# Optimization experiments

Hardware: AMD Instinct MI355X
Metric: run time of the kernel (lower is better)

## Reference

```python
import jax, jax.numpy as jnp
import numpy as np

N = 100000      # nodes
E = 3200000     # edges (avg degree 32)
F_IN = 256      # n_features
HID = 128       # n_hidden
C = 16          # n_classes
K = 10          # propagation hops


def setup_inputs() -> dict:
    key = jax.random.key(0)
    ks = jax.random.split(key, 12)
    x = jax.random.normal(ks[0], (N, F_IN), jnp.float32)
    edge_index = jax.random.randint(ks[1], (2, E), 0, N, dtype=jnp.int64)
    edge_attr = jax.random.uniform(ks[2], (E,), jnp.float32)
    # learned parameters (torch Linear layout: W [out, in], b [out])
    def lin(k, fan_out, fan_in):
        s = 1.0 / np.sqrt(fan_in)
        kw, kb = jax.random.split(k)
        W = jax.random.uniform(kw, (fan_out, fan_in), jnp.float32, -s, s)
        b = jax.random.uniform(kb, (fan_out,), jnp.float32, -s, s)
        return W, b
    lin1_w, lin1_b = lin(ks[3], HID, F_IN)
    lin2_w, lin2_b = lin(ks[4], HID, HID)   # hidden lin (n_layers-3 == 1)
    lin3_w, lin3_b = lin(ks[5], C, HID)     # classes lin
    proj_w, proj_b = lin(ks[6], 1, C)       # Prop retain-score projection
    return {"x": x, "edge_index": edge_index, "edge_attr": edge_attr,
            "lin1_w": lin1_w, "lin1_b": lin1_b,
            "lin2_w": lin2_w, "lin2_b": lin2_b,
            "lin3_w": lin3_w, "lin3_b": lin3_b,
            "proj_w": proj_w, "proj_b": proj_b}


def reference(x, edge_index, edge_attr,
              lin1_w, lin1_b, lin2_w, lin2_b, lin3_w, lin3_b,
              proj_w, proj_b):
    # MLP stack (dropout is identity in eval mode)
    h = jax.nn.relu(x @ lin1_w.T + lin1_b)
    h = jax.nn.relu(h @ lin2_w.T + lin2_b)
    h = jax.nn.relu(h @ lin3_w.T + lin3_b)          # [N, C]

    src, dst = edge_index[0], edge_index[1]
    norm = edge_attr[:, None]                        # [E, 1]

    def hop(carry, _):
        msg = norm * carry[src]                      # gather + scale [E, C]
        nxt = jax.ops.segment_sum(msg, dst, num_segments=N)  # scatter-add
        return nxt, nxt

    _, hops = jax.lax.scan(hop, h, None, length=K)   # [K, N, C]
    pps = jnp.concatenate([h[None], hops], axis=0)   # [K+1, N, C]
    pps = jnp.transpose(pps, (1, 0, 2))              # [N, K+1, C]

    # adaptive combination: sigmoid(Linear(C->1)) per hop, weighted sum
    score = jax.nn.sigmoid(jnp.einsum('nkc,c->nk', pps, proj_w[0]) + proj_b[0])
    out = jnp.einsum('nk,nkc->nc', score, pps)       # [N, C]
    return out
```

## Files before the change

kernel.cpp:

```cpp
#include <hip/hip_runtime.h>
#include <hip/hip_bf16.h>
#include <math.h>

#define N_NODES 100000
#define E_EDGES 3200000
#define K_HOPS  10
#define NPP     256
#define NPART   ((N_NODES + NPP - 1) / NPP)
#define CHUNK   4096
#define EPT     (CHUNK / 256)
#define NCHUNK  ((E_EDGES + CHUNK - 1) / CHUNK)
#define NFLAT   (NPART * NCHUNK)
#define SSEG    8192
#define GA      ((NFLAT + SSEG - 1) / SSEG)

typedef __attribute__((ext_vector_type(8))) short short8;
typedef __attribute__((ext_vector_type(4))) float floatx4;

__device__ __forceinline__ ushort f2bf(float f) {
    uint u = __float_as_uint(f);
    u += 0x7fffu + ((u >> 16) & 1u);
    return (ushort)(u >> 16);
}
__device__ __forceinline__ uint pk2(float a, float b) {
    return (uint)f2bf(a) | ((uint)f2bf(b) << 16);
}
__device__ __forceinline__ float bflo(uint u) { return __uint_as_float(u << 16); }
__device__ __forceinline__ float bfhi(uint u) { return __uint_as_float(u & 0xffff0000u); }

template<int KD, int MD, bool A_F32>
__global__ __launch_bounds__(256) void mfma_mlp(
    const void* __restrict__ Av, const float* __restrict__ W,
    const float* __restrict__ bias, ushort* __restrict__ C)
{
    constexpr int NCT = MD / 16;
    constexpr int LDW = 88;
    __shared__ ushort Wl[MD * LDW];

    const int t    = threadIdx.x;
    const int w    = t >> 6;
    const int lane = t & 63;
    const int m    = lane & 15;
    const int quad = lane >> 4;
    const int rowBase = blockIdx.x * 128 + w * 32;

    floatx4 acc[2][NCT];
#pragma unroll
    for (int rt = 0; rt < 2; ++rt)
#pragma unroll
        for (int ct = 0; ct < NCT; ++ct) acc[rt][ct] = (floatx4)0.f;

    for (int kb = 0; kb < KD; kb += 64) {
#pragma unroll
        for (int j = 0; j < MD / 16; ++j) {
            int flat = j * 256 + t;
            int n  = flat >> 4;
            int c4 = (flat & 15) * 4;
            floatx4 v = *(const floatx4*)&W[(size_t)n * KD + kb + c4];
            *(uint2*)&Wl[n * LDW + c4] = make_uint2(pk2(v[0], v[1]), pk2(v[2], v[3]));
        }
        __syncthreads();
#pragma unroll
        for (int ks = 0; ks < 64; ks += 32) {
            short8 af[2];
#pragma unroll
            for (int rt = 0; rt < 2; ++rt) {
                int row = rowBase + rt * 16 + m;
                row = row < N_NODES ? row : N_NODES - 1;
                size_t base = (size_t)row * KD + kb + ks + quad * 8;
                if constexpr (A_F32) {
                    const float* ap = (const float*)Av + base;
                    floatx4 a0 = *(const floatx4*)ap;
                    floatx4 a1 = *(const floatx4*)(ap + 4);
                    short8 x;
                    x[0] = (short)f2bf(a0[0]); x[1] = (short)f2bf(a0[1]);
                    x[2] = (short)f2bf(a0[2]); x[3] = (short)f2bf(a0[3]);
                    x[4] = (short)f2bf(a1[0]); x[5] = (short)f2bf(a1[1]);
                    x[6] = (short)f2bf(a1[2]); x[7] = (short)f2bf(a1[3]);
                    af[rt] = x;
                } else {
                    af[rt] = *(const short8*)((const ushort*)Av + base);
                }
            }
#pragma unroll
            for (int ct = 0; ct < NCT; ++ct) {
                short8 bf = *(const short8*)&Wl[(ct * 16 + m) * LDW + ks + quad * 8];
#pragma unroll
                for (int rt = 0; rt < 2; ++rt)
                    acc[rt][ct] = __builtin_amdgcn_mfma_f32_16x16x32_bf16(
                        af[rt], bf, acc[rt][ct], 0, 0, 0);
            }
        }
        __syncthreads();
    }

#pragma unroll
    for (int rt = 0; rt < 2; ++rt) {
#pragma unroll
        for (int r = 0; r < 4; ++r) {
            int row = rowBase + rt * 16 + quad * 4 + r;
            if (row < N_NODES) {
#pragma unroll
                for (int ct = 0; ct < NCT; ++ct) {
                    int col = ct * 16 + m;
                    float v = acc[rt][ct][r] + bias[col];
                    v = v > 0.f ? v : 0.f;
                    C[(size_t)row * MD + col] = f2bf(v);
                }
            }
        }
    }
}

__global__ __launch_bounds__(256) void hist2(
    const int* __restrict__ dst, int* __restrict__ cmat)
{
    __shared__ int lhist[NPART];
    const int t = threadIdx.x;
    for (int p = t; p < NPART; p += 256) lhist[p] = 0;
    __syncthreads();
    const int base = blockIdx.x * CHUNK;
#pragma unroll
    for (int j = 0; j < EPT; ++j) {
        int i = base + j * 256 + t;
        if (i < E_EDGES) atomicAdd(&lhist[dst[i] >> 8], 1);
    }
    __syncthreads();
    for (int p = t; p < NPART; p += 256)
        cmat[p * NCHUNK + blockIdx.x] = lhist[p];
}

__global__ __launch_bounds__(1024) void scan_reduce(
    const int* __restrict__ cmat, int* __restrict__ bsum)
{
    __shared__ int wsum[16];
    const int t = threadIdx.x, lane = t & 63, wid = t >> 6;
    int base = blockIdx.x * SSEG + t * 8;
    int s = 0;
#pragma unroll
    for (int j = 0; j < 8; ++j) {
        int idx = base + j;
        if (idx < NFLAT) s += cmat[idx];
    }
#pragma unroll
    for (int d = 1; d < 64; d <<= 1) s += __shfl_xor(s, d);
    if (lane == 0) wsum[wid] = s;
    __syncthreads();
    if (t == 0) {
        int tot = 0;
#pragma unroll
        for (int i = 0; i < 16; ++i) tot += wsum[i];
        bsum[blockIdx.x] = tot;
    }
}

__global__ void scan_tops(const int* __restrict__ bsum, int* __restrict__ boff)
{
    const int t = threadIdx.x;
    int v = (t < GA) ? bsum[t] : 0;
    int x = v;
#pragma unroll
    for (int d = 1; d < 64; d <<= 1) {
        int y = __shfl_up(x, d);
        if (t >= d) x += y;
    }
    if (t < GA) boff[t] = x - v;
}

__global__ __launch_bounds__(1024) void scan_apply(
    int* __restrict__ cmat, const int* __restrict__ boff, int* __restrict__ pbase)
{
    __shared__ int wsum[16];
    __shared__ int woff[17];
    const int t = threadIdx.x, lane = t & 63, wid = t >> 6;
    int base = blockIdx.x * SSEG + t * 8;
    int v[8], pre[8];
    int s = 0;
#pragma unroll
    for (int j = 0; j < 8; ++j) {
        int idx = base + j;
        v[j] = (idx < NFLAT) ? cmat[idx] : 0;
        pre[j] = s;
        s += v[j];
    }
    int x = s;
#pragma unroll
    for (int d = 1; d < 64; d <<= 1) {
        int y = __shfl_up(x, d);
        if (lane >= d) x += y;
    }
    if (lane == 63) wsum[wid] = x;
    __syncthreads();
    if (wid == 0) {
        int w = (lane < 16) ? wsum[lane] : 0;
#pragma unroll
        for (int d = 1; d < 16; d <<= 1) {
            int y = __shfl_up(w, d);
            if (lane >= d) w += y;
        }
        if (lane < 16) woff[lane + 1] = w;
        if (lane == 0) woff[0] = 0;
    }
    __syncthreads();
    int tbase = boff[blockIdx.x] + woff[wid] + (x - s);
#pragma unroll
    for (int j = 0; j < 8; ++j) {
        int idx = base + j;
        if (idx < NFLAT) {
            int e = tbase + pre[j];
            cmat[idx] = e;
            if (idx % NCHUNK == 0) pbase[idx / NCHUNK] = e;
        }
    }
    if (blockIdx.x == 0 && t == 0) pbase[NPART] = E_EDGES;
}

__global__ __launch_bounds__(256) void scatter2(
    const int* __restrict__ src, const int* __restrict__ dst,
    const float* __restrict__ ea, const int* __restrict__ cbase,
    int2* __restrict__ staging)
{
    __shared__ int lcur[NPART];
    const int t = threadIdx.x;
    const int b = blockIdx.x;
    for (int p = t; p < NPART; p += 256) lcur[p] = cbase[p * NCHUNK + b];
    __syncthreads();
    const int base = b * CHUNK;

    int d[EPT], pos[EPT];
#pragma unroll
    for (int j = 0; j < EPT; ++j) {
        int i = base + j * 256 + t;
        d[j] = (i < E_EDGES) ? dst[i] : -1;
    }
#pragma unroll
    for (int j = 0; j < EPT; ++j) {
        if (d[j] >= 0) pos[j] = atomicAdd(&lcur[d[j] >> 8], 1);
    }
#pragma unroll
    for (int j = 0; j < EPT; ++j) {
        if (d[j] >= 0) {
            int i = base + j * 256 + t;
            staging[pos[j]] = make_int2(__float_as_int(ea[i]),
                                        src[i] | ((d[j] & 255) << 17));
        }
    }
}

__global__ __launch_bounds__(1024) void partition_build(
    const int2* __restrict__ staging, const int* __restrict__ pbase,
    int* __restrict__ rowp, int2* __restrict__ csr)
{
    __shared__ int ncnt[NPP];
    __shared__ int wsum[4];
    const int p = blockIdx.x;
    const int t = threadIdx.x;
    const int e0 = pbase[p], e1 = pbase[p + 1];
    const int cnt = e1 - e0;
    const int n0 = p << 8;

    if (t < NPP) ncnt[t] = 0;
    __syncthreads();
    for (int e = t; e < cnt; e += 1024)
        atomicAdd(&ncnt[(staging[e0 + e].y >> 17) & 255], 1);
    __syncthreads();

    int x = 0, v = 0;
    if (t < NPP) {
        const int lane = t & 63, wid = t >> 6;
        v = ncnt[t];
        x = v;
#pragma unroll
        for (int d = 1; d < 64; d <<= 1) {
            int y = __shfl_up(x, d);
            if (lane >= d) x += y;
        }
        if (lane == 63) wsum[wid] = x;
    }
    __syncthreads();
    if (t < NPP) {
        const int wid = t >> 6;
        int wbase = 0;
#pragma unroll
        for (int w = 0; w < 4; ++w) if (w < wid) wbase += wsum[w];
        int excl = wbase + x - v;
        ncnt[t] = e0 + excl;
        int n = n0 + t;
        if (n < N_NODES) rowp[n] = e0 + excl;
    }
    if (p == NPART - 1 && t == 0) rowp[N_NODES] = E_EDGES;
    __syncthreads();

    for (int e = t; e < cnt; e += 1024) {
        int2 en = staging[e0 + e];
        int dlo = (en.y >> 17) & 255;
        int pos = atomicAdd(&ncnt[dlo], 1);
        csr[pos] = make_int2(en.y & 0x1FFFF, en.x);
    }
}

__global__ __launch_bounds__(256) void init_out_bf16(
    const ushort* __restrict__ h, const float* __restrict__ pw,
    const float* __restrict__ pb, float* __restrict__ out)
{
    const int t = threadIdx.x;
    const int l = t & 1;
    const int n = blockIdx.x * 128 + (t >> 1);
    if (n >= N_NODES) return;
    uint4 v = *(const uint4*)&h[(size_t)n * 16 + l * 8];
    float a0 = bflo(v.x), a1 = bfhi(v.x), a2 = bflo(v.y), a3 = bfhi(v.y);
    float a4 = bflo(v.z), a5 = bfhi(v.z), a6 = bflo(v.w), a7 = bfhi(v.w);
    float4 p0 = ((const float4*)pw)[l * 2];
    float4 p1 = ((const float4*)pw)[l * 2 + 1];
    float part = a0 * p0.x + a1 * p0.y + a2 * p0.z + a3 * p0.w
               + a4 * p1.x + a5 * p1.y + a6 * p1.z + a7 * p1.w;
    part += __shfl_xor(part, 1);
    float s = 1.f / (1.f + __expf(-(part + pb[0])));
    *(float4*)&out[(size_t)n * 16 + l * 8]     = make_float4(s*a0, s*a1, s*a2, s*a3);
    *(float4*)&out[(size_t)n * 16 + l * 8 + 4] = make_float4(s*a4, s*a5, s*a6, s*a7);
}

__global__ __launch_bounds__(256) void hop_bf16(
    const ushort* __restrict__ prev, ushort* __restrict__ next,
    const int* __restrict__ rowp, const int2* __restrict__ csr,
    const float* __restrict__ pw, const float* __restrict__ pb,
    float* __restrict__ out)
{
    const int t = threadIdx.x;
    const int l = t & 1;
    const int g = (t >> 1) & 3;
    const int n = blockIdx.x * 32 + (t >> 3);
    if (n >= N_NODES) return;
    const int e0 = rowp[n], e1 = rowp[n + 1];
    float a[8];
#pragma unroll
    for (int j = 0; j < 8; ++j) a[j] = 0.f;

    int e = e0 + g;
    for (; e + 4 < e1; e += 8) {
        int2 c0 = csr[e];
        int2 c1 = csr[e + 4];
        float w0 = __int_as_float(c0.y);
        float w1 = __int_as_float(c1.y);
        uint4 v0 = *(const uint4*)&prev[(size_t)c0.x * 16 + l * 8];
        uint4 v1 = *(const uint4*)&prev[(size_t)c1.x * 16 + l * 8];
        a[0] += w0 * bflo(v0.x); a[1] += w0 * bfhi(v0.x);
        a[2] += w0 * bflo(v0.y); a[3] += w0 * bfhi(v0.y);
        a[4] += w0 * bflo(v0.z); a[5] += w0 * bfhi(v0.z);
        a[6] += w0 * bflo(v0.w); a[7] += w0 * bfhi(v0.w);
        a[0] += w1 * bflo(v1.x); a[1] += w1 * bfhi(v1.x);
        a[2] += w1 * bflo(v1.y); a[3] += w1 * bfhi(v1.y);
        a[4] += w1 * bflo(v1.z); a[5] += w1 * bfhi(v1.z);
        a[6] += w1 * bflo(v1.w); a[7] += w1 * bfhi(v1.w);
    }
    if (e < e1) {
        int2 c0 = csr[e];
        float w0 = __int_as_float(c0.y);
        uint4 v0 = *(const uint4*)&prev[(size_t)c0.x * 16 + l * 8];
        a[0] += w0 * bflo(v0.x); a[1] += w0 * bfhi(v0.x);
        a[2] += w0 * bflo(v0.y); a[3] += w0 * bfhi(v0.y);
        a[4] += w0 * bflo(v0.z); a[5] += w0 * bfhi(v0.z);
        a[6] += w0 * bflo(v0.w); a[7] += w0 * bfhi(v0.w);
    }

#pragma unroll
    for (int d = 2; d <= 4; d <<= 1) {
#pragma unroll
        for (int j = 0; j < 8; ++j) a[j] += __shfl_xor(a[j], d);
    }

    float4 p0 = ((const float4*)pw)[l * 2];
    float4 p1 = ((const float4*)pw)[l * 2 + 1];
    float part = a[0]*p0.x + a[1]*p0.y + a[2]*p0.z + a[3]*p0.w
               + a[4]*p1.x + a[5]*p1.y + a[6]*p1.z + a[7]*p1.w;
    part += __shfl_xor(part, 1);
    float s = 1.f / (1.f + __expf(-(part + pb[0])));

    if (g == 0) {
        uint4 nv = make_uint4(pk2(a[0], a[1]), pk2(a[2], a[3]),
                              pk2(a[4], a[5]), pk2(a[6], a[7]));
        *(uint4*)&next[(size_t)n * 16 + l * 8] = nv;
        float4 o0 = *(float4*)&out[(size_t)n * 16 + l * 8];
        float4 o1 = *(float4*)&out[(size_t)n * 16 + l * 8 + 4];
        o0.x += s*a[0]; o0.y += s*a[1]; o0.z += s*a[2]; o0.w += s*a[3];
        o1.x += s*a[4]; o1.y += s*a[5]; o1.z += s*a[6]; o1.w += s*a[7];
        *(float4*)&out[(size_t)n * 16 + l * 8]     = o0;
        *(float4*)&out[(size_t)n * 16 + l * 8 + 4] = o1;
    }
}

extern "C" void kernel_launch(void* const* d_in, const int* in_sizes, int n_in,
                              void* d_out, int out_size, void* d_ws, size_t ws_size,
                              hipStream_t stream)
{
    const float* x  = (const float*)d_in[0];
    const int*   ei = (const int*)d_in[1];
    const float* ea = (const float*)d_in[2];
    const float* w1 = (const float*)d_in[3];
    const float* b1 = (const float*)d_in[4];
    const float* w2 = (const float*)d_in[5];
    const float* b2 = (const float*)d_in[6];
    const float* w3 = (const float*)d_in[7];
    const float* b3 = (const float*)d_in[8];
    const float* pw = (const float*)d_in[9];
    const float* pb = (const float*)d_in[10];
    float* out = (float*)d_out;

    char* ws = (char*)d_ws;
    size_t off = 0;
    char*   region0 = ws + off;           off += (size_t)E_EDGES * 16;
    ushort* pingb = (ushort*)(ws + off);  off += (size_t)N_NODES * 16 * 2;
    ushort* pongb = (ushort*)(ws + off);  off += (size_t)N_NODES * 16 * 2;
    int*    rowp  = (int*)(ws + off);     off += (((size_t)(N_NODES + 1) * 4) + 15) & ~(size_t)15;
    int*    cmat  = (int*)(ws + off);     off += ((size_t)NFLAT * 4 + 15) & ~(size_t)15;
    int*    bsum  = (int*)(ws + off);     off += ((size_t)GA * 4 + 15) & ~(size_t)15;
    int*    boff  = (int*)(ws + off);     off += ((size_t)GA * 4 + 15) & ~(size_t)15;
    int*    pbase = (int*)(ws + off);     off += ((size_t)(NPART + 1) * 4 + 15) & ~(size_t)15;
    int2*   csr   = (int2*)(ws + off);    off += (size_t)E_EDGES * 8;

    int2*   staging = (int2*)region0;
    ushort* h1b = (ushort*)region0;
    ushort* h2b = (ushort*)(region0 + (size_t)N_NODES * 128 * 2);

    const int* src = ei;
    const int* dst = ei + E_EDGES;

    const dim3 blk(256);
    const int mlpGrid    = (N_NODES + 127) / 128;
    const int hopGrid    = (N_NODES + 31) / 32;

    hist2<<<NCHUNK, blk, 0, stream>>>(dst, cmat);
    scan_reduce<<<GA, 1024, 0, stream>>>(cmat, bsum);
    scan_tops<<<1, 64, 0, stream>>>(bsum, boff);
    scan_apply<<<GA, 1024, 0, stream>>>(cmat, boff, pbase);
    scatter2<<<NCHUNK, blk, 0, stream>>>(src, dst, ea, cmat, staging);
    partition_build<<<NPART, 1024, 0, stream>>>(staging, pbase, rowp, csr);

    mfma_mlp<256, 128, true ><<<mlpGrid, blk, 0, stream>>>(x,   w1, b1, h1b);
    mfma_mlp<128, 128, false><<<mlpGrid, blk, 0, stream>>>(h1b, w2, b2, h2b);
    mfma_mlp<128,  16, false><<<mlpGrid, blk, 0, stream>>>(h2b, w3, b3, pingb);

    init_out_bf16<<<mlpGrid, blk, 0, stream>>>(pingb, pw, pb, out);

    const ushort* prev = pingb;
    ushort* next = pongb;
    for (int k = 0; k < K_HOPS; ++k) {
        hop_bf16<<<hopGrid, blk, 0, stream>>>(prev, next, rowp, csr, pw, pb, out);
        ushort* tmp = (ushort*)prev; prev = next; next = tmp;
    }
}
```

Baseline: 641.1 us.

## Stage per-chunk edges in shared memory for coalesced scatter; unroll hop gathers

The edge scatter kernel now counting-sorts each 4096-edge chunk by destination partition in shared memory, then writes the staging array in a linear pass. This replaces scattered per-edge global writes with mostly contiguous runs. The hop kernel's gather loop is unrolled to keep four neighbor loads in flight per thread group, with a loop for the remainder. The cost is about 50KB of shared memory per scatter block, which reduces occupancy, plus extra syncs and a prefix scan.

```diff
diff --git a/kernel.cpp b/kernel.cpp
--- a/kernel.cpp
+++ b/kernel.cpp
@@ -215,36 +215,74 @@
     if (blockIdx.x == 0 && t == 0) pbase[NPART] = E_EDGES;
 }
 
-__global__ __launch_bounds__(256) void scatter2(
+__global__ __launch_bounds__(256) void scatter3(
     const int* __restrict__ src, const int* __restrict__ dst,
     const float* __restrict__ ea, const int* __restrict__ cbase,
     int2* __restrict__ staging)
 {
-    __shared__ int lcur[NPART];
+    __shared__ int2 ebuf[CHUNK];
+    __shared__ int  gaddr[CHUNK];
+    __shared__ int  lcnt[NPART];
+    __shared__ int  goff[NPART];
+    __shared__ int  wsum[4];
     const int t = threadIdx.x;
     const int b = blockIdx.x;
-    for (int p = t; p < NPART; p += 256) lcur[p] = cbase[p * NCHUNK + b];
-    __syncthreads();
     const int base = b * CHUNK;
-
-    int d[EPT], pos[EPT];
+    const int cnt = min(CHUNK, E_EDGES - base);
+    const int lane = t & 63, wid = t >> 6;
+
+    for (int p = t; p < NPART; p += 256) lcnt[p] = 0;
+    __syncthreads();
+
+    int d[EPT];
 #pragma unroll
     for (int j = 0; j < EPT; ++j) {
         int i = base + j * 256 + t;
         d[j] = (i < E_EDGES) ? dst[i] : -1;
-    }
-#pragma unroll
-    for (int j = 0; j < EPT; ++j) {
-        if (d[j] >= 0) pos[j] = atomicAdd(&lcur[d[j] >> 8], 1);
-    }
+        if (d[j] >= 0) atomicAdd(&lcnt[d[j] >> 8], 1);
+    }
+    __syncthreads();
+
+    int v0 = (2 * t     < NPART) ? lcnt[2 * t]     : 0;
+    int v1 = (2 * t + 1 < NPART) ? lcnt[2 * t + 1] : 0;
+    int pair = v0 + v1;
+    int x = pair;
+#pragma unroll
+    for (int dd = 1; dd < 64; dd <<= 1) {
+        int y = __shfl_up(x, dd);
+        if (lane >= dd) x += y;
+    }
+    if (lane == 63) wsum[wid] = x;
+    __syncthreads();
+    int wbase = 0;
+#pragma unroll
+    for (int w = 0; w < 4; ++w) if (w < wid) wbase += wsum[w];
+    int excl = wbase + x - pair;
+    if (2 * t < NPART) {
+        lcnt[2 * t] = excl;
+        goff[2 * t] = cbase[(2 * t) * NCHUNK + b] - excl;
+    }
+    if (2 * t + 1 < NPART) {
+        lcnt[2 * t + 1] = excl + v0;
+        goff[2 * t + 1] = cbase[(2 * t + 1) * NCHUNK + b] - (excl + v0);
+    }
+    __syncthreads();
+
 #pragma unroll
     for (int j = 0; j < EPT; ++j) {
         if (d[j] >= 0) {
             int i = base + j * 256 + t;
-            staging[pos[j]] = make_int2(__float_as_int(ea[i]),
-                                        src[i] | ((d[j] & 255) << 17));
-        }
-    }
+            int p = d[j] >> 8;
+            int s = atomicAdd(&lcnt[p], 1);
+            ebuf[s]  = make_int2(__float_as_int(ea[i]),
+                                 src[i] | ((d[j] & 255) << 17));
+            gaddr[s] = goff[p] + s;
+        }
+    }
+    __syncthreads();
+
+    for (int k = t; k < cnt; k += 256)
+        staging[gaddr[k]] = ebuf[k];
 }
 
 __global__ __launch_bounds__(1024) void partition_build(
@@ -337,13 +375,17 @@
     for (int j = 0; j < 8; ++j) a[j] = 0.f;
 
     int e = e0 + g;
-    for (; e + 4 < e1; e += 8) {
+    for (; e + 12 < e1; e += 16) {
         int2 c0 = csr[e];
         int2 c1 = csr[e + 4];
-        float w0 = __int_as_float(c0.y);
-        float w1 = __int_as_float(c1.y);
+        int2 c2 = csr[e + 8];
+        int2 c3 = csr[e + 12];
+        float w0 = __int_as_float(c0.y), w1 = __int_as_float(c1.y);
+        float w2 = __int_as_float(c2.y), w3 = __int_as_float(c3.y);
         uint4 v0 = *(const uint4*)&prev[(size_t)c0.x * 16 + l * 8];
         uint4 v1 = *(const uint4*)&prev[(size_t)c1.x * 16 + l * 8];
+        uint4 v2 = *(const uint4*)&prev[(size_t)c2.x * 16 + l * 8];
+        uint4 v3 = *(const uint4*)&prev[(size_t)c3.x * 16 + l * 8];
         a[0] += w0 * bflo(v0.x); a[1] += w0 * bfhi(v0.x);
         a[2] += w0 * bflo(v0.y); a[3] += w0 * bfhi(v0.y);
         a[4] += w0 * bflo(v0.z); a[5] += w0 * bfhi(v0.z);
@@ -352,8 +394,16 @@
         a[2] += w1 * bflo(v1.y); a[3] += w1 * bfhi(v1.y);
         a[4] += w1 * bflo(v1.z); a[5] += w1 * bfhi(v1.z);
         a[6] += w1 * bflo(v1.w); a[7] += w1 * bfhi(v1.w);
-    }
-    if (e < e1) {
+        a[0] += w2 * bflo(v2.x); a[1] += w2 * bfhi(v2.x);
+        a[2] += w2 * bflo(v2.y); a[3] += w2 * bfhi(v2.y);
+        a[4] += w2 * bflo(v2.z); a[5] += w2 * bfhi(v2.z);
+        a[6] += w2 * bflo(v2.w); a[7] += w2 * bfhi(v2.w);
+        a[0] += w3 * bflo(v3.x); a[1] += w3 * bfhi(v3.x);
+        a[2] += w3 * bflo(v3.y); a[3] += w3 * bfhi(v3.y);
+        a[4] += w3 * bflo(v3.z); a[5] += w3 * bfhi(v3.z);
+        a[6] += w3 * bflo(v3.w); a[7] += w3 * bfhi(v3.w);
+    }
+    for (; e < e1; e += 4) {
         int2 c0 = csr[e];
         float w0 = __int_as_float(c0.y);
         uint4 v0 = *(const uint4*)&prev[(size_t)c0.x * 16 + l * 8];
@@ -433,7 +483,7 @@
     scan_reduce<<<GA, 1024, 0, stream>>>(cmat, bsum);
     scan_tops<<<1, 64, 0, stream>>>(bsum, boff);
     scan_apply<<<GA, 1024, 0, stream>>>(cmat, boff, pbase);
-    scatter2<<<NCHUNK, blk, 0, stream>>>(src, dst, ea, cmat, staging);
+    scatter3<<<NCHUNK, blk, 0, stream>>>(src, dst, ea, cmat, staging);
     partition_build<<<NPART, 1024, 0, stream>>>(staging, pbase, rowp, csr);
 
     mfma_mlp<256, 128, true ><<<mlpGrid, blk, 0, stream>>>(x,   w1, b1, h1b);
```

Result: faster. 596.3 us (-7.0%).
